# Performance work log

Hardware: AMD Instinct MI355X
Metric: run time of the kernel (lower is better)

Reference implementation:

```python
import jax, jax.numpy as jnp
import numpy as np

B, IN_DIM, OUT_DIM = 262144, 2, 256


def setup_inputs() -> dict:
    key = jax.random.key(0)
    k1, k2, k3 = jax.random.split(key, 3)
    x = jax.random.normal(k1, (B, IN_DIM), dtype=jnp.float32)
    h = jax.random.normal(k2, (OUT_DIM, IN_DIM), dtype=jnp.float32) * 0.01
    delta = jax.random.normal(k3, (OUT_DIM,), dtype=jnp.float32) * 0.01
    return {"x": x, "h": h, "delta": delta}


def reference(x, h, delta):
    # z = F.linear(x, h): [B, OUT_DIM]
    theta = x @ h.T + delta  # phase argument, delta broadcast over batch
    out_real = jnp.cos(theta)
    out_imag = jnp.sin(theta)
    # S_proxy = diag_embed(mean_b out_complex); eigvals of a diagonal matrix
    # are its diagonal entries, so angles are arctan2(mean_imag, mean_real).
    mean_r = out_real.mean(axis=0)  # [OUT_DIM]
    mean_i = out_imag.mean(axis=0)  # [OUT_DIM]
    eta = jnp.sum(jnp.arctan2(mean_i, mean_r)) / jnp.pi
    return out_real, eta
```

## Files before the change

### kernel.cpp

```cpp
#include <hip/hip_runtime.h>
#include <math.h>


#define B_DIM 262144
#define O_DIM 256
#define NB1 1024
#define NB2 64

typedef float vf4 __attribute__((ext_vector_type(4)));

__global__ __launch_bounds__(256) void fdc_main(
    const float* __restrict__ x, const float* __restrict__ h,
    const float* __restrict__ delta, float* __restrict__ out,
    float* __restrict__ partial ) {
  const int tid  = threadIdx.x;
  const int lane = tid & 63;
  const int rl   = tid >> 6;
  const int col4 = lane * 4;

  const float4* h4 = (const float4*)h;
  const float4 ha = h4[lane * 2];
  const float4 hb = h4[lane * 2 + 1];
  const float4 dl = ((const float4*)delta)[lane];

  const float2* x2 = (const float2*)x;
  vf4* out4 = (vf4*)out;

  float sc0 = 0.f, sc1 = 0.f, sc2 = 0.f, sc3 = 0.f;
  float ss0 = 0.f, ss1 = 0.f, ss2 = 0.f, ss3 = 0.f;

  const int stride = NB1 * 8;
  for (int base = blockIdx.x * 8 + rl * 2; base < B_DIM; base += stride) {
#pragma unroll
    for (int k = 0; k < 2; ++k) {
      const int row = base + k;
      const float2 xv = x2[row];
      float s, c;
      vf4 o;
      const float t0 = fmaf(xv.x, ha.x, fmaf(xv.y, ha.y, dl.x));
      const float t1 = fmaf(xv.x, ha.z, fmaf(xv.y, ha.w, dl.y));
      const float t2 = fmaf(xv.x, hb.x, fmaf(xv.y, hb.y, dl.z));
      const float t3 = fmaf(xv.x, hb.z, fmaf(xv.y, hb.w, dl.w));
      __sincosf(t0, &s, &c); o.x = c; sc0 += c; ss0 += s;
      __sincosf(t1, &s, &c); o.y = c; sc1 += c; ss1 += s;
      __sincosf(t2, &s, &c); o.z = c; sc2 += c; ss2 += s;
      __sincosf(t3, &s, &c); o.w = c; sc3 += c; ss3 += s;
      __builtin_nontemporal_store(o, &out4[(size_t)row * 64 + lane]);
    }
  }

  __shared__ float lds[4][512];
  lds[rl][col4 + 0] = sc0; lds[rl][col4 + 1] = sc1;
  lds[rl][col4 + 2] = sc2; lds[rl][col4 + 3] = sc3;
  lds[rl][256 + col4 + 0] = ss0; lds[rl][256 + col4 + 1] = ss1;
  lds[rl][256 + col4 + 2] = ss2; lds[rl][256 + col4 + 3] = ss3;
  __syncthreads();
  const float a = lds[0][tid] + lds[1][tid] + lds[2][tid] + lds[3][tid];
  const float b = lds[0][tid + 256] + lds[1][tid + 256] +
                  lds[2][tid + 256] + lds[3][tid + 256];
  float* p = partial + (size_t)blockIdx.x * 512;
  p[tid] = a;
  p[256 + tid] = b;
}

__global__ __launch_bounds__(256) void fdc_red1(
    const float* __restrict__ partial, float* __restrict__ partial2) {
  const int t = threadIdx.x;
  const float* base = partial + (size_t)blockIdx.x * (NB1 / NB2) * 512;
  float cs = 0.f, sn = 0.f;
#pragma unroll
  for (int r = 0; r < NB1 / NB2; ++r) {
    cs += base[r * 512 + t];
    sn += base[r * 512 + 256 + t];
  }
  partial2[(size_t)blockIdx.x * 512 + t] = cs;
  partial2[(size_t)blockIdx.x * 512 + 256 + t] = sn;
}

__global__ __launch_bounds__(256) void fdc_red2(
    const float* __restrict__ partial2, float* __restrict__ out) {
  const int t = threadIdx.x;
  float cs = 0.f, sn = 0.f;
#pragma unroll 4
  for (int r = 0; r < NB2; ++r) {
    cs += partial2[(size_t)r * 512 + t];
    sn += partial2[(size_t)r * 512 + 256 + t];
  }
  float ang = atan2f(sn, cs);
  __shared__ float red[256];
  red[t] = ang;
  __syncthreads();
  for (int st = 128; st > 0; st >>= 1) {
    if (t < st) red[t] += red[t + st];
    __syncthreads();
  }
  if (t == 0) out[(size_t)B_DIM * O_DIM] = red[0] * (float)(1.0 / M_PI);
}

extern "C" void kernel_launch(void* const* d_in, const int* in_sizes, int n_in,
                              void* d_out, int out_size, void* d_ws, size_t ws_size,
                              hipStream_t stream) {
  const float* x     = (const float*)d_in[0];
  const float* h     = (const float*)d_in[1];
  const float* delta = (const float*)d_in[2];
  float* out = (float*)d_out;
  float* partial  = (float*)d_ws;
  float* partial2 = partial + (size_t)NB1 * 512;
  (void)ws_size;

  fdc_main<<<NB1, 256, 0, stream>>>(x, h, delta, out, partial);
  fdc_red1<<<NB2, 256, 0, stream>>>(partial, partial2);
  fdc_red2<<<1, 256, 0, stream>>>(partial2, out);
}
```

Measured before the change: 287.5 us.

## Stage x rows in LDS and give each wave a contiguous row range

Each block now owns a contiguous chunk of 128 rows and loads that chunk's x values cooperatively into shared memory with one coalesced read, replacing the per-row uniform global loads. Each wave then processes 32 consecutive rows, so its output stores form a contiguous region. The grid doubles to 2048 blocks, which also doubles the partial-sum workspace and the work in the first reduction stage. The kernel is dominated by the 256 MB output write, so the expected effect is small, and it adds a barrier before compute starts.

```diff
diff --git a/kernel.cpp b/kernel.cpp
--- a/kernel.cpp
+++ b/kernel.cpp
@@ -4,8 +4,10 @@
 
 #define B_DIM 262144
 #define O_DIM 256
-#define NB1 1024
+#define NB1 2048
 #define NB2 64
+#define ROWS_PER_BLOCK (B_DIM / NB1)
+#define ROWS_PER_WAVE (ROWS_PER_BLOCK / 4)
 
 typedef float vf4 __attribute__((ext_vector_type(4)));
 
@@ -15,7 +17,7 @@
     float* __restrict__ partial ) {
   const int tid  = threadIdx.x;
   const int lane = tid & 63;
-  const int rl   = tid >> 6;
+  const int wv   = tid >> 6;
   const int col4 = lane * 4;
 
   const float4* h4 = (const float4*)h;
@@ -23,37 +25,38 @@
   const float4 hb = h4[lane * 2 + 1];
   const float4 dl = ((const float4*)delta)[lane];
 
-  const float2* x2 = (const float2*)x;
+  __shared__ float2 xs[ROWS_PER_BLOCK];
+  ((float*)xs)[tid] = x[(size_t)blockIdx.x * (ROWS_PER_BLOCK * 2) + tid];
+  __syncthreads();
+
   vf4* out4 = (vf4*)out;
-
   float sc0 = 0.f, sc1 = 0.f, sc2 = 0.f, sc3 = 0.f;
   float ss0 = 0.f, ss1 = 0.f, ss2 = 0.f, ss3 = 0.f;
 
-  const int stride = NB1 * 8;
-  for (int base = blockIdx.x * 8 + rl * 2; base < B_DIM; base += stride) {
-#pragma unroll
-    for (int k = 0; k < 2; ++k) {
-      const int row = base + k;
-      const float2 xv = x2[row];
-      float s, c;
-      vf4 o;
-      const float t0 = fmaf(xv.x, ha.x, fmaf(xv.y, ha.y, dl.x));
-      const float t1 = fmaf(xv.x, ha.z, fmaf(xv.y, ha.w, dl.y));
-      const float t2 = fmaf(xv.x, hb.x, fmaf(xv.y, hb.y, dl.z));
-      const float t3 = fmaf(xv.x, hb.z, fmaf(xv.y, hb.w, dl.w));
-      __sincosf(t0, &s, &c); o.x = c; sc0 += c; ss0 += s;
-      __sincosf(t1, &s, &c); o.y = c; sc1 += c; ss1 += s;
-      __sincosf(t2, &s, &c); o.z = c; sc2 += c; ss2 += s;
-      __sincosf(t3, &s, &c); o.w = c; sc3 += c; ss3 += s;
-      __builtin_nontemporal_store(o, &out4[(size_t)row * 64 + lane]);
-    }
+  const int rbase = blockIdx.x * ROWS_PER_BLOCK + wv * ROWS_PER_WAVE;
+  const int lbase = wv * ROWS_PER_WAVE;
+#pragma unroll 4
+  for (int i = 0; i < ROWS_PER_WAVE; ++i) {
+    const float2 xv = xs[lbase + i];
+    const int row = rbase + i;
+    float s, c;
+    vf4 o;
+    const float t0 = fmaf(xv.x, ha.x, fmaf(xv.y, ha.y, dl.x));
+    const float t1 = fmaf(xv.x, ha.z, fmaf(xv.y, ha.w, dl.y));
+    const float t2 = fmaf(xv.x, hb.x, fmaf(xv.y, hb.y, dl.z));
+    const float t3 = fmaf(xv.x, hb.z, fmaf(xv.y, hb.w, dl.w));
+    __sincosf(t0, &s, &c); o.x = c; sc0 += c; ss0 += s;
+    __sincosf(t1, &s, &c); o.y = c; sc1 += c; ss1 += s;
+    __sincosf(t2, &s, &c); o.z = c; sc2 += c; ss2 += s;
+    __sincosf(t3, &s, &c); o.w = c; sc3 += c; ss3 += s;
+    __builtin_nontemporal_store(o, &out4[(size_t)row * 64 + lane]);
   }
 
   __shared__ float lds[4][512];
-  lds[rl][col4 + 0] = sc0; lds[rl][col4 + 1] = sc1;
-  lds[rl][col4 + 2] = sc2; lds[rl][col4 + 3] = sc3;
-  lds[rl][256 + col4 + 0] = ss0; lds[rl][256 + col4 + 1] = ss1;
-  lds[rl][256 + col4 + 2] = ss2; lds[rl][256 + col4 + 3] = ss3;
+  lds[wv][col4 + 0] = sc0; lds[wv][col4 + 1] = sc1;
+  lds[wv][col4 + 2] = sc2; lds[wv][col4 + 3] = sc3;
+  lds[wv][256 + col4 + 0] = ss0; lds[wv][256 + col4 + 1] = ss1;
+  lds[wv][256 + col4 + 2] = ss2; lds[wv][256 + col4 + 3] = ss3;
   __syncthreads();
   const float a = lds[0][tid] + lds[1][tid] + lds[2][tid] + lds[3][tid];
   const float b = lds[0][tid + 256] + lds[1][tid + 256] +
@@ -68,7 +71,7 @@
   const int t = threadIdx.x;
   const float* base = partial + (size_t)blockIdx.x * (NB1 / NB2) * 512;
   float cs = 0.f, sn = 0.f;
-#pragma unroll
+#pragma unroll 8
   for (int r = 0; r < NB1 / NB2; ++r) {
     cs += base[r * 512 + t];
     sn += base[r * 512 + 256 + t];
```

Result: faster. 277.3 us (-3.6%).
